# Kernel tuning notes

Hardware: AMD Instinct MI355X
Metric: run time of the kernel (lower is better)

## Reference

```python
import jax, jax.numpy as jnp
import numpy as np

B, C, W, H = 32, 512, 28, 28  # input spatial = 2*init_width x 2*init_height
HEADS = 8


def setup_inputs() -> dict:
    key = jax.random.key(0)
    ks = jax.random.split(key, 9)
    d = C // HEADS
    s = 0.05
    return {
        "x": jax.random.normal(ks[0], (B, C, W, H), jnp.float32),
        # 1x1 conv weights == dense [out_c, in_c] + bias
        "wq": jax.random.normal(ks[1], (C, C), jnp.float32) * s,
        "bq": jax.random.normal(ks[2], (C,), jnp.float32) * s,
        "wk": jax.random.normal(ks[3], (C, C), jnp.float32) * s,
        "bk": jax.random.normal(ks[4], (C,), jnp.float32) * s,
        "wv": jax.random.normal(ks[5], (C, C), jnp.float32) * s,
        "bv": jax.random.normal(ks[6], (C,), jnp.float32) * s,
        "rel_h": jax.random.normal(ks[7], (1, HEADS, d, 1, H), jnp.float32),
        "rel_w": jax.random.normal(ks[8], (1, HEADS, d, W, 1), jnp.float32),
    }


def reference(x, wq, bq, wk, bk, wv, bv, rel_h, rel_w):
    b, c, w, h = x.shape
    heads = rel_h.shape[1]
    d = c // heads
    n = w * h

    def proj(wt, bi):
        # 1x1 conv == per-pixel dense over channels
        y = jnp.einsum('oc,bcwh->bowh', wt, x) + bi[None, :, None, None]
        return y.reshape(b, heads, d, n)  # [B, H, d, N]

    q = proj(wq, bq)
    k = proj(wk, bk)
    v = proj(wv, bv)

    # content-content: q^T k -> [B, H, N, N]
    cc = jnp.einsum('bhdn,bhdm->bhnm', q, k)
    # relative position bias: (rel_h + rel_w) broadcast to [H, d, 2w0*2h0] = [H, d, N]
    pos = (rel_h + rel_w).reshape(heads, d, n)
    # content-position: pos^T @ q -> [B, H, N, N]
    cp = jnp.einsum('hdp,bhdn->bhpn', pos, q)

    attn = jax.nn.softmax(cc + cp, axis=-1)  # softmax over last dim
    # out = v @ attn^T : [B, H, d, N]
    out = jnp.einsum('bhdn,bhmn->bhdm', v, attn)
    return out.reshape(b, c, w, h)
```

## Files before the change

### kernel.cpp

```cpp
#include <hip/hip_runtime.h>


#define BATCH 32
#define CCH   512
#define NHEAD 8
#define DH    64
#define NTOK  784
#define WSP   28
#define OT    64
#define NT    112
#define WLD   40
#define CH    64
#define NCHUNK 13
#define KQLD  136
#define VLD   72

typedef unsigned short u16;
typedef unsigned int   u32;
typedef short  short8  __attribute__((ext_vector_type(8)));
typedef float  floatx4 __attribute__((ext_vector_type(4)));

__device__ __forceinline__ u16 f2bf(float f) {
    union { float f; u32 i; } v; v.f = f;
    u32 x = v.i;
    return (u16)((x + 0x7FFFu + ((x >> 16) & 1u)) >> 16);
}
__device__ __forceinline__ u32 f2u(float f) { union { float f; u32 i; } v; v.f = f; return v.i; }
__device__ __forceinline__ float u2f(u32 u) { union { u32 i; float f; } v; v.i = u; return v.f; }

__device__ __forceinline__ u32 packsplit(float f) {
    const u32 hib = f2u(f) & 0xFFFF0000u;
    const float lo = f - u2f(hib);
    return ((u32)f2bf(lo) << 16) | (hib >> 16);
}

__global__ __launch_bounds__(256)
void pack_weights(const float* __restrict__ wq, const float* __restrict__ wk,
                  const float* __restrict__ wv,
                  u32* __restrict__ Wqp, u32* __restrict__ Wkp, u32* __restrict__ Wvp)
{
    const int i = blockIdx.x * 256 + threadIdx.x;
    if (i < CCH * CCH) {
        Wqp[i] = packsplit(wq[i]);
        Wkp[i] = packsplit(wk[i]);
        Wvp[i] = packsplit(wv[i]);
    }
}

__global__ __launch_bounds__(256)
void pack_x(const float* __restrict__ x, u32* __restrict__ Xp, int b0, size_t count)
{
    const size_t i = (size_t)blockIdx.x * 256 + threadIdx.x;
    if (i < count)
        Xp[i] = packsplit(x[(size_t)b0 * CCH * NTOK + i]);
}

__global__ __launch_bounds__(256)
void qkv_proj(const u32* __restrict__ Xp,
              const u32* __restrict__ Wqp, const float* __restrict__ bq,
              const u32* __restrict__ Wkp, const float* __restrict__ bk,
              const u32* __restrict__ Wvp, const float* __restrict__ bv,
              u32* __restrict__ Qp, u32* __restrict__ Kp, u16* __restrict__ Vo,
              int nbatch)
{
    const int t    = threadIdx.x;
    const int lane = t & 63;
    const int wid  = t >> 6;
    const int z    = blockIdx.z;
    const int proj = z / nbatch;
    const int bl   = z - proj * nbatch;
    const int o0   = blockIdx.y * OT;
    const int n0   = blockIdx.x * NT;

    const u32*   Wp   = (proj == 0) ? Wqp : (proj == 1) ? Wkp : Wvp;
    const float* bias = (proj == 0) ? bq  : (proj == 1) ? bk  : bv;

    __shared__ u16 wh[OT][WLD], wl[OT][WLD];
    __shared__ u16 xh[NT][WLD], xl[NT][WLD];

    const int m    = lane & 15;
    const int quad = lane >> 4;

    floatx4 acc[7];
    #pragma unroll
    for (int j = 0; j < 7; j++) acc[j] = (floatx4){0.f, 0.f, 0.f, 0.f};

    const int wo = t >> 2;
    const int wc = (t & 3) * 8;
    const int xc = t >> 3;
    const int xn = (t & 7) * 14;

    const size_t xbase = (size_t)bl * CCH * NTOK;

    for (int c0 = 0; c0 < CCH; c0 += 32) {
        uint4 wv0 = *reinterpret_cast<const uint4*>(&Wp[(size_t)(o0 + wo) * CCH + c0 + wc]);
        uint4 wv1 = *reinterpret_cast<const uint4*>(&Wp[(size_t)(o0 + wo) * CCH + c0 + wc + 4]);
        u32 xreg[14];
        #pragma unroll
        for (int u = 0; u < 7; u++) {
            const uint2 p = *reinterpret_cast<const uint2*>(&Xp[xbase + (size_t)(c0 + xc) * NTOK + n0 + xn + 2 * u]);
            xreg[2 * u] = p.x; xreg[2 * u + 1] = p.y;
        }
        __syncthreads();
        {
            const u32 wr[8] = {wv0.x, wv0.y, wv0.z, wv0.w, wv1.x, wv1.y, wv1.z, wv1.w};
            ushort4 h0 = make_ushort4((u16)(wr[0] & 0xFFFF), (u16)(wr[1] & 0xFFFF), (u16)(wr[2] & 0xFFFF), (u16)(wr[3] & 0xFFFF));
            ushort4 h1 = make_ushort4((u16)(wr[4] & 0xFFFF), (u16)(wr[5] & 0xFFFF), (u16)(wr[6] & 0xFFFF), (u16)(wr[7] & 0xFFFF));
            ushort4 l0 = make_ushort4((u16)(wr[0] >> 16), (u16)(wr[1] >> 16), (u16)(wr[2] >> 16), (u16)(wr[3] >> 16));
            ushort4 l1 = make_ushort4((u16)(wr[4] >> 16), (u16)(wr[5] >> 16), (u16)(wr[6] >> 16), (u16)(wr[7] >> 16));
            *reinterpret_cast<ushort4*>(&wh[wo][wc])     = h0;
            *reinterpret_cast<ushort4*>(&wh[wo][wc + 4]) = h1;
            *reinterpret_cast<ushort4*>(&wl[wo][wc])     = l0;
            *reinterpret_cast<ushort4*>(&wl[wo][wc + 4]) = l1;
        }
        #pragma unroll
        for (int u = 0; u < 14; u++) {
            xh[xn + u][xc] = (u16)(xreg[u] & 0xFFFFu);
            xl[xn + u][xc] = (u16)(xreg[u] >> 16);
        }
        __syncthreads();

        const short8 Ah = *reinterpret_cast<const short8*>(&wh[wid * 16 + m][quad * 8]);
        const short8 Al = *reinterpret_cast<const short8*>(&wl[wid * 16 + m][quad * 8]);
        #pragma unroll
        for (int jt = 0; jt < 7; jt++) {
            const short8 Bh = *reinterpret_cast<const short8*>(&xh[jt * 16 + m][quad * 8]);
            const short8 Bl = *reinterpret_cast<const short8*>(&xl[jt * 16 + m][quad * 8]);
            acc[jt] = __builtin_amdgcn_mfma_f32_16x16x32_bf16(Ah, Bh, acc[jt], 0, 0, 0);
            acc[jt] = __builtin_amdgcn_mfma_f32_16x16x32_bf16(Ah, Bl, acc[jt], 0, 0, 0);
            acc[jt] = __builtin_amdgcn_mfma_f32_16x16x32_bf16(Al, Bh, acc[jt], 0, 0, 0);
        }
    }

    const size_t obase = (size_t)bl * CCH * NTOK;
    #pragma unroll
    for (int r = 0; r < 4; r++) {
        const int o = o0 + wid * 16 + quad * 4 + r;
        const float bi = bias[o];
        #pragma unroll
        for (int jt = 0; jt < 7; jt++) {
            const int n = n0 + jt * 16 + m;
            const float val = acc[jt][r] + bi;
            const size_t idx = obase + (size_t)o * NTOK + n;
            if (proj == 0)      Qp[idx] = packsplit(val);
            else if (proj == 1) Kp[idx] = packsplit(val);
            else                Vo[idx] = f2bf(val);
        }
    }
}

__global__ __launch_bounds__(256)
void attn_kernel(const u32* __restrict__ Qp, const u32* __restrict__ Kp,
                 const u16* __restrict__ V,
                 const float* __restrict__ rel_h, const float* __restrict__ rel_w,
                 float* __restrict__ out, int b0)
{
    const int t    = threadIdx.x;
    const int lane = t & 63;
    const int wid  = t >> 6;
    const int m    = lane & 15;
    const int quad = lane >> 4;
    int i0 = blockIdx.x * 64;
    if (i0 > NTOK - 64) i0 = NTOK - 64;
    const int h  = blockIdx.y;
    const int bl = blockIdx.z;
    const int b  = b0 + bl;
    const int hd = h * DH;
    const size_t base  = ((size_t)bl * CCH + hd) * NTOK;
    const size_t baseo = ((size_t)b  * CCH + hd) * NTOK;

    __shared__ u16 kqh[CH][KQLD];
    __shared__ u16 kql[CH][KQLD];
    __shared__ u16 vt[DH][VLD];
    __shared__ u16 pt[64][VLD];

    short8 Bh[4], Bl[4];
    {
        const int ig = i0 + wid * 16 + m;
        const int iw = ig / WSP, ih = ig % WSP;
        #pragma unroll
        for (int c = 0; c < 4; c++) {
            union { short8 v; u16 u[8]; } hb, lb;
            #pragma unroll
            for (int idx = 0; idx < 8; idx++) {
                const int k = c * 32 + quad * 8 + idx;
                if (k < DH) {
                    const u32 p = Qp[base + (size_t)k * NTOK + ig];
                    hb.u[idx] = (u16)(p & 0xFFFFu);
                    lb.u[idx] = (u16)(p >> 16);
                } else {
                    const int d = k - DH;
                    const float pos = rel_h[(size_t)(hd + d) * WSP + ih]
                                    + rel_w[(size_t)(hd + d) * WSP + iw];
                    const u32 hib = f2u(pos) & 0xFFFF0000u;
                    hb.u[idx] = (u16)(hib >> 16);
                    lb.u[idx] = f2bf(pos - u2f(hib));
                }
            }
            Bh[c] = hb.v; Bl[c] = lb.v;
        }
    }

    floatx4 Oacc[4];
    #pragma unroll
    for (int dt = 0; dt < 4; dt++) Oacc[dt] = (floatx4){0.f, 0.f, 0.f, 0.f};
    float mrun = -1e30f, lrun = 0.f;

    const int cg = t & 31, c0 = cg * 4;
    const int jg = t >> 5, jb = jg * 8;
    const int vd = t >> 2, vj = (t & 3) * 16;

    for (int chn = 0; chn < NCHUNK; chn++) {
        const int j0 = chn * CH;
        __syncthreads();

        {
            u32 kv[4][8];
            #pragma unroll
            for (int cc = 0; cc < 4; cc++) {
                const int c = c0 + cc;
                const u32* src = (c < DH) ? (Kp + base + (size_t)c * NTOK)
                                          : (Qp + base + (size_t)(c - DH) * NTOK);
                const uint4 a  = *reinterpret_cast<const uint4*>(&src[j0 + jb]);
                const uint4 a2 = *reinterpret_cast<const uint4*>(&src[j0 + jb + 4]);
                kv[cc][0] = a.x;  kv[cc][1] = a.y;  kv[cc][2] = a.z;  kv[cc][3] = a.w;
                kv[cc][4] = a2.x; kv[cc][5] = a2.y; kv[cc][6] = a2.z; kv[cc][7] = a2.w;
            }
            #pragma unroll
            for (int jj = 0; jj < 8; jj++) {
                const ushort4 hi = make_ushort4((u16)(kv[0][jj] & 0xFFFFu), (u16)(kv[1][jj] & 0xFFFFu),
                                                (u16)(kv[2][jj] & 0xFFFFu), (u16)(kv[3][jj] & 0xFFFFu));
                const ushort4 lo = make_ushort4((u16)(kv[0][jj] >> 16), (u16)(kv[1][jj] >> 16),
                                                (u16)(kv[2][jj] >> 16), (u16)(kv[3][jj] >> 16));
                *reinterpret_cast<ushort4*>(&kqh[jb + jj][c0]) = hi;
                *reinterpret_cast<ushort4*>(&kql[jb + jj][c0]) = lo;
            }
        }
        if (j0 + vj + 16 <= NTOK) {
            const uint4 a  = *reinterpret_cast<const uint4*>(&V[base + (size_t)vd * NTOK + j0 + vj]);
            const uint4 a2 = *reinterpret_cast<const uint4*>(&V[base + (size_t)vd * NTOK + j0 + vj + 8]);
            *reinterpret_cast<uint4*>(&vt[vd][vj])     = a;
            *reinterpret_cast<uint4*>(&vt[vd][vj + 8]) = a2;
        } else {
            #pragma unroll
            for (int u = 0; u < 16; u++)
                vt[vd][vj + u] = (j0 + vj + u < NTOK) ? V[base + (size_t)vd * NTOK + j0 + vj + u] : (u16)0;
        }
        __syncthreads();

        floatx4 Sacc[4];
        #pragma unroll
        for (int js = 0; js < 4; js++) Sacc[js] = (floatx4){0.f, 0.f, 0.f, 0.f};
        #pragma unroll
        for (int c = 0; c < 4; c++) {
            #pragma unroll
            for (int js = 0; js < 4; js++) {
                const short8 Ah = *reinterpret_cast<const short8*>(&kqh[js * 16 + m][c * 32 + quad * 8]);
                const short8 Al = *reinterpret_cast<const short8*>(&kql[js * 16 + m][c * 32 + quad * 8]);
                Sacc[js] = __builtin_amdgcn_mfma_f32_16x16x32_bf16(Ah, Bh[c], Sacc[js], 0, 0, 0);
                Sacc[js] = __builtin_amdgcn_mfma_f32_16x16x32_bf16(Ah, Bl[c], Sacc[js], 0, 0, 0);
                Sacc[js] = __builtin_amdgcn_mfma_f32_16x16x32_bf16(Al, Bh[c], Sacc[js], 0, 0, 0);
            }
        }

        float sv[16];
        #pragma unroll
        for (int js = 0; js < 4; js++)
            #pragma unroll
            for (int r = 0; r < 4; r++) sv[js * 4 + r] = Sacc[js][r];
        if (j0 + CH > NTOK) {
            #pragma unroll
            for (int js = 0; js < 4; js++)
                #pragma unroll
                for (int r = 0; r < 4; r++)
                    if (j0 + js * 16 + quad * 4 + r >= NTOK) sv[js * 4 + r] = -1e30f;
        }
        float mc = sv[0];
        #pragma unroll
        for (int u = 1; u < 16; u++) mc = fmaxf(mc, sv[u]);
        mc = fmaxf(mc, __shfl_xor(mc, 16, 64));
        mc = fmaxf(mc, __shfl_xor(mc, 32, 64));
        const float mnew  = fmaxf(mrun, mc);
        const float alpha = __expf(mrun - mnew);
        float ps = 0.f;
        #pragma unroll
        for (int u = 0; u < 16; u++) {
            const float p = __expf(sv[u] - mnew);
            sv[u] = p;
            ps += p;
        }
        ps += __shfl_xor(ps, 16, 64);
        ps += __shfl_xor(ps, 32, 64);
        lrun = lrun * alpha + ps;
        mrun = mnew;
        #pragma unroll
        for (int dt = 0; dt < 4; dt++)
            #pragma unroll
            for (int r = 0; r < 4; r++) Oacc[dt][r] *= alpha;

        #pragma unroll
        for (int js = 0; js < 4; js++) {
            const ushort4 pw = make_ushort4(f2bf(sv[js * 4 + 0]), f2bf(sv[js * 4 + 1]),
                                            f2bf(sv[js * 4 + 2]), f2bf(sv[js * 4 + 3]));
            *reinterpret_cast<ushort4*>(&pt[wid * 16 + m][js * 16 + quad * 4]) = pw;
        }

        #pragma unroll
        for (int joff = 0; joff < CH; joff += 32) {
            const short8 Bp = *reinterpret_cast<const short8*>(&pt[wid * 16 + m][joff + quad * 8]);
            #pragma unroll
            for (int dt = 0; dt < 4; dt++) {
                const short8 Av = *reinterpret_cast<const short8*>(&vt[dt * 16 + m][joff + quad * 8]);
                Oacc[dt] = __builtin_amdgcn_mfma_f32_16x16x32_bf16(Av, Bp, Oacc[dt], 0, 0, 0);
            }
        }
    }

    const float linv = 1.f / lrun;
    #pragma unroll
    for (int dt = 0; dt < 4; dt++) {
        #pragma unroll
        for (int r = 0; r < 4; r++) {
            const int d = dt * 16 + quad * 4 + r;
            out[baseo + (size_t)d * NTOK + i0 + wid * 16 + m] = Oacc[dt][r] * linv;
        }
    }
}

extern "C" void kernel_launch(void* const* d_in, const int* in_sizes, int n_in,
                              void* d_out, int out_size, void* d_ws, size_t ws_size,
                              hipStream_t stream)
{
    const float* x  = (const float*)d_in[0];
    const float* wq = (const float*)d_in[1];
    const float* bq = (const float*)d_in[2];
    const float* wk = (const float*)d_in[3];
    const float* bk = (const float*)d_in[4];
    const float* wv = (const float*)d_in[5];
    const float* bv = (const float*)d_in[6];
    const float* rh = (const float*)d_in[7];
    const float* rw = (const float*)d_in[8];
    float* out = (float*)d_out;

    const size_t perB = (size_t)CCH * NTOK;
    const size_t WELEM = (size_t)CCH * CCH;
    const size_t weightBytes = 3 * WELEM * 4;
    const size_t perBatchBytes = perB * 14;

    size_t avail = (ws_size > weightBytes) ? (ws_size - weightBytes) : perBatchBytes;
    size_t nb_s = avail / perBatchBytes;
    int nb = (int)(nb_s < 1 ? 1 : (nb_s > BATCH ? BATCH : nb_s));

    u32* Wqp = (u32*)d_ws;
    u32* Wkp = Wqp + WELEM;
    u32* Wvp = Wkp + WELEM;
    u32* chunk0 = Wvp + WELEM;

    pack_weights<<<dim3((CCH * CCH + 255) / 256), dim3(256), 0, stream>>>(wq, wk, wv, Wqp, Wkp, Wvp);

    for (int b0 = 0; b0 < BATCH; b0 += nb) {
        const int curb = (BATCH - b0 < nb) ? (BATCH - b0) : nb;
        u32* Xp = chunk0;
        u32* Qp = Xp + (size_t)curb * perB;
        u32* Kp = Qp + (size_t)curb * perB;
        u16* Vb = (u16*)(Kp + (size_t)curb * perB);

        const size_t xcount = (size_t)curb * perB;
        pack_x<<<dim3((unsigned)((xcount + 255) / 256)), dim3(256), 0, stream>>>(x, Xp, b0, xcount);

        dim3 gp(NTOK / NT, CCH / OT, 3 * curb);
        qkv_proj<<<gp, dim3(256), 0, stream>>>(Xp, Wqp, bq, Wkp, bk, Wvp, bv,
                                               Qp, Kp, Vb, curb);

        dim3 ga(NCHUNK, NHEAD, curb);
        attn_kernel<<<ga, dim3(256), 0, stream>>>(Qp, Kp, Vb, rh, rw, out, b0);
    }
}
```

Before: 604.1 us.

## Double per-block tiles to 512 threads in projection and attention kernels

The QKV projection now uses 128 output channels per block with 512 threads, and only the first 256 threads load the X tile, so each staged X tile is reused across twice as many output rows. The attention kernel processes 128 queries per block with 512 threads. Each K/Q/V chunk staged in shared memory now serves twice as many query rows, and the grid is reordered so batch varies fastest. This halves redundant K/V global loads and staging work, at the cost of fewer, larger blocks, more duplicated work on the clamped last query tile (784 is not a multiple of 128), and possible occupancy or register pressure.

```diff
diff --git a/kernel.cpp b/kernel.cpp
--- a/kernel.cpp
+++ b/kernel.cpp
@@ -7,11 +7,12 @@
 #define DH    64
 #define NTOK  784
 #define WSP   28
-#define OT    64
+#define OT    128
 #define NT    112
 #define WLD   40
 #define CH    64
 #define NCHUNK 13
+#define NIBLK  7
 #define KQLD  136
 #define VLD   72
 
@@ -55,7 +56,7 @@
         Xp[i] = packsplit(x[(size_t)b0 * CCH * NTOK + i]);
 }
 
-__global__ __launch_bounds__(256)
+__global__ __launch_bounds__(512)
 void qkv_proj(const u32* __restrict__ Xp,
               const u32* __restrict__ Wqp, const float* __restrict__ bq,
               const u32* __restrict__ Wkp, const float* __restrict__ bk,
@@ -96,10 +97,12 @@
         uint4 wv0 = *reinterpret_cast<const uint4*>(&Wp[(size_t)(o0 + wo) * CCH + c0 + wc]);
         uint4 wv1 = *reinterpret_cast<const uint4*>(&Wp[(size_t)(o0 + wo) * CCH + c0 + wc + 4]);
         u32 xreg[14];
-        #pragma unroll
-        for (int u = 0; u < 7; u++) {
-            const uint2 p = *reinterpret_cast<const uint2*>(&Xp[xbase + (size_t)(c0 + xc) * NTOK + n0 + xn + 2 * u]);
-            xreg[2 * u] = p.x; xreg[2 * u + 1] = p.y;
+        if (t < 256) {
+            #pragma unroll
+            for (int u = 0; u < 7; u++) {
+                const uint2 p = *reinterpret_cast<const uint2*>(&Xp[xbase + (size_t)(c0 + xc) * NTOK + n0 + xn + 2 * u]);
+                xreg[2 * u] = p.x; xreg[2 * u + 1] = p.y;
+            }
         }
         __syncthreads();
         {
@@ -113,10 +116,12 @@
             *reinterpret_cast<ushort4*>(&wl[wo][wc])     = l0;
             *reinterpret_cast<ushort4*>(&wl[wo][wc + 4]) = l1;
         }
-        #pragma unroll
-        for (int u = 0; u < 14; u++) {
-            xh[xn + u][xc] = (u16)(xreg[u] & 0xFFFFu);
-            xl[xn + u][xc] = (u16)(xreg[u] >> 16);
+        if (t < 256) {
+            #pragma unroll
+            for (int u = 0; u < 14; u++) {
+                xh[xn + u][xc] = (u16)(xreg[u] & 0xFFFFu);
+                xl[xn + u][xc] = (u16)(xreg[u] >> 16);
+            }
         }
         __syncthreads();
 
@@ -149,7 +154,7 @@
     }
 }
 
-__global__ __launch_bounds__(256)
+__global__ __launch_bounds__(512)
 void attn_kernel(const u32* __restrict__ Qp, const u32* __restrict__ Kp,
                  const u16* __restrict__ V,
                  const float* __restrict__ rel_h, const float* __restrict__ rel_w,
@@ -160,10 +165,10 @@
     const int wid  = t >> 6;
     const int m    = lane & 15;
     const int quad = lane >> 4;
-    int i0 = blockIdx.x * 64;
-    if (i0 > NTOK - 64) i0 = NTOK - 64;
-    const int h  = blockIdx.y;
-    const int bl = blockIdx.z;
+    const int bl   = blockIdx.x;
+    const int h    = blockIdx.y;
+    int i0 = blockIdx.z * 128;
+    if (i0 > NTOK - 128) i0 = NTOK - 128;
     const int b  = b0 + bl;
     const int hd = h * DH;
     const size_t base  = ((size_t)bl * CCH + hd) * NTOK;
@@ -172,7 +177,7 @@
     __shared__ u16 kqh[CH][KQLD];
     __shared__ u16 kql[CH][KQLD];
     __shared__ u16 vt[DH][VLD];
-    __shared__ u16 pt[64][VLD];
+    __shared__ u16 pt[128][VLD];
 
     short8 Bh[4], Bl[4];
     {
@@ -206,44 +211,41 @@
     for (int dt = 0; dt < 4; dt++) Oacc[dt] = (floatx4){0.f, 0.f, 0.f, 0.f};
     float mrun = -1e30f, lrun = 0.f;
 
-    const int cg = t & 31, c0 = cg * 4;
-    const int jg = t >> 5, jb = jg * 8;
-    const int vd = t >> 2, vj = (t & 3) * 16;
+    const int cg4 = (t & 31) * 4;
+    const int jb4 = (t >> 5) * 4;
+    const int vd  = t >> 3;
+    const int vj  = (t & 7) * 8;
 
     for (int chn = 0; chn < NCHUNK; chn++) {
         const int j0 = chn * CH;
         __syncthreads();
 
         {
-            u32 kv[4][8];
+            u32 kv[4][4];
             #pragma unroll
             for (int cc = 0; cc < 4; cc++) {
-                const int c = c0 + cc;
+                const int c = cg4 + cc;
                 const u32* src = (c < DH) ? (Kp + base + (size_t)c * NTOK)
                                           : (Qp + base + (size_t)(c - DH) * NTOK);
-                const uint4 a  = *reinterpret_cast<const uint4*>(&src[j0 + jb]);
-                const uint4 a2 = *reinterpret_cast<const uint4*>(&src[j0 + jb + 4]);
-                kv[cc][0] = a.x;  kv[cc][1] = a.y;  kv[cc][2] = a.z;  kv[cc][3] = a.w;
-                kv[cc][4] = a2.x; kv[cc][5] = a2.y; kv[cc][6] = a2.z; kv[cc][7] = a2.w;
-            }
-            #pragma unroll
-            for (int jj = 0; jj < 8; jj++) {
+                const uint4 a = *reinterpret_cast<const uint4*>(&src[j0 + jb4]);
+                kv[cc][0] = a.x; kv[cc][1] = a.y; kv[cc][2] = a.z; kv[cc][3] = a.w;
+            }
+            #pragma unroll
+            for (int jj = 0; jj < 4; jj++) {
                 const ushort4 hi = make_ushort4((u16)(kv[0][jj] & 0xFFFFu), (u16)(kv[1][jj] & 0xFFFFu),
                                                 (u16)(kv[2][jj] & 0xFFFFu), (u16)(kv[3][jj] & 0xFFFFu));
                 const ushort4 lo = make_ushort4((u16)(kv[0][jj] >> 16), (u16)(kv[1][jj] >> 16),
                                                 (u16)(kv[2][jj] >> 16), (u16)(kv[3][jj] >> 16));
-                *reinterpret_cast<ushort4*>(&kqh[jb + jj][c0]) = hi;
-                *reinterpret_cast<ushort4*>(&kql[jb + jj][c0]) = lo;
-            }
-        }
-        if (j0 + vj + 16 <= NTOK) {
-            const uint4 a  = *reinterpret_cast<const uint4*>(&V[base + (size_t)vd * NTOK + j0 + vj]);
-            const uint4 a2 = *reinterpret_cast<const uint4*>(&V[base + (size_t)vd * NTOK + j0 + vj + 8]);
-            *reinterpret_cast<uint4*>(&vt[vd][vj])     = a;
-            *reinterpret_cast<uint4*>(&vt[vd][vj + 8]) = a2;
+                *reinterpret_cast<ushort4*>(&kqh[jb4 + jj][cg4]) = hi;
+                *reinterpret_cast<ushort4*>(&kql[jb4 + jj][cg4]) = lo;
+            }
+        }
+        if (j0 + vj + 8 <= NTOK) {
+            const uint4 a = *reinterpret_cast<const uint4*>(&V[base + (size_t)vd * NTOK + j0 + vj]);
+            *reinterpret_cast<uint4*>(&vt[vd][vj]) = a;
         } else {
             #pragma unroll
-            for (int u = 0; u < 16; u++)
+            for (int u = 0; u < 8; u++)
                 vt[vd][vj + u] = (j0 + vj + u < NTOK) ? V[base + (size_t)vd * NTOK + j0 + vj + u] : (u16)0;
         }
         __syncthreads();
@@ -369,10 +371,10 @@
         pack_x<<<dim3((unsigned)((xcount + 255) / 256)), dim3(256), 0, stream>>>(x, Xp, b0, xcount);
 
         dim3 gp(NTOK / NT, CCH / OT, 3 * curb);
-        qkv_proj<<<gp, dim3(256), 0, stream>>>(Xp, Wqp, bq, Wkp, bk, Wvp, bv,
+        qkv_proj<<<gp, dim3(512), 0, stream>>>(Xp, Wqp, bq, Wkp, bk, Wvp, bv,
                                                Qp, Kp, Vb, curb);
 
-        dim3 ga(NCHUNK, NHEAD, curb);
-        attn_kernel<<<ga, dim3(256), 0, stream>>>(Qp, Kp, Vb, rh, rw, out, b0);
-    }
-}
+        dim3 ga(curb, NHEAD, NIBLK);
+        attn_kernel<<<ga, dim3(512), 0, stream>>>(Qp, Kp, Vb, rh, rw, out, b0);
+    }
+}
```

Result: faster. 531.9 us (-11.9%).
